# Kernel tuning notes

Measured on AMD Instinct MI355X. Metric: run time of the kernel, lower is better.

The kernel has to match this reference:

```python
import jax, jax.numpy as jnp
import numpy as np

N, IN_F, OUT_F = 8192, 512, 64
ALPHA = 0.2  # LeakyReLU negative slope


def setup_inputs() -> dict:
    key = jax.random.key(0)
    k1, k2, k3, k4 = jax.random.split(key, 4)
    x = jax.random.normal(k1, (N, IN_F), dtype=jnp.float32)
    # dense 0/1 adjacency; Bernoulli(0.5) so every row has neighbors
    adj = jax.random.randint(k2, (N, N), 0, 2, dtype=jnp.int32)
    # W stored as [in, out] (torch Linear applies x @ W.T; equivalent math)
    W = jax.random.normal(k3, (IN_F, OUT_F), dtype=jnp.float32) / np.sqrt(IN_F)
    a = jax.random.normal(k4, (2 * OUT_F,), dtype=jnp.float32) * 0.1
    return {"x": x, "adj": adj, "W": W, "a": a}


def reference(x, adj, W, a):
    # Wh: [n, out]
    Wh = x @ W
    # concat([Wh_i, Wh_j]) @ a  ==  (Wh @ a1)_i + (Wh @ a2)_j  (split 'a' in halves)
    a1, a2 = a[:OUT_F], a[OUT_F:]
    e = (Wh @ a1)[:, None] + (Wh @ a2)[None, :]          # [n, n]
    e = jnp.where(e > 0, e, ALPHA * e)                    # LeakyReLU
    e = jnp.where(adj == 0, -jnp.inf, e)                  # mask non-edges
    attn = jax.nn.softmax(e, axis=1)                      # softmax over neighbors j
    # dropout omitted: eval mode (training=False)
    return attn @ Wh                                      # [n, out]
```

## Files before the change

### kernel.cpp

```cpp
#include <hip/hip_runtime.h>
#include <cstdint>
#include <cstddef>

#define NN 8192
#define INF 512
#define OUTF 64
#define ALPHA 0.2f
#define NSPLIT 16
#define JSPLIT (NN / NSPLIT)
#define NW32 (NN / 32)
#define GEMM_BLOCKS 512

typedef short bf16x8 __attribute__((ext_vector_type(8)));
typedef float f32x4 __attribute__((ext_vector_type(4)));

static __device__ inline unsigned short f2bf(float f) {
    unsigned u = __builtin_bit_cast(unsigned, f);
    unsigned r = (u + 0x7FFFu + ((u >> 16) & 1u)) >> 16;
    return (unsigned short)r;
}

__global__ __launch_bounds__(256) void k01_fused(
    const float* __restrict__ x, const int* __restrict__ adj,
    const float* __restrict__ W, const float* __restrict__ a,
    unsigned short* __restrict__ Asw, float* __restrict__ U,
    float* __restrict__ E2p, float* __restrict__ E2n,
    unsigned* __restrict__ mask)
{
    __shared__ int ldsbuf[8192];
    const int tid = threadIdx.x;

    if (blockIdx.x >= GEMM_BLOCKS) {
        const int row = blockIdx.x - GEMM_BLOCKS;
        const int* arow = adj + (size_t)row * NN;

        #pragma unroll
        for (int k = 0; k < 8; ++k) {
            const int i = k * 1024 + tid * 4;
            int4 v = *(const int4*)(arow + i);
            const int p = i ^ (((i >> 7) & 7) << 2);
            *(int4*)&ldsbuf[p] = v;
        }
        __syncthreads();

        unsigned m = 0;
        #pragma unroll
        for (int k = 0; k < 8; ++k) {
            const int i2 = tid * 32 + k * 4;
            const int p2 = i2 ^ (((i2 >> 7) & 7) << 2);
            int4 v = *(const int4*)&ldsbuf[p2];
            m |= (v.x != 0 ? 1u : 0u) << (4 * k);
            m |= (v.y != 0 ? 1u : 0u) << (4 * k + 1);
            m |= (v.z != 0 ? 1u : 0u) << (4 * k + 2);
            m |= (v.w != 0 ? 1u : 0u) << (4 * k + 3);
        }
        mask[(size_t)row * NW32 + tid] = m;
        return;
    }

    const int i0 = blockIdx.x * 16;
    const int w  = __builtin_amdgcn_readfirstlane(tid >> 6);
    const int c  = tid & 63;

    const float* xr = x + (size_t)(i0 + 4 * w) * INF;
    const float* Wc = W + c;
    float acc[4] = {0.f, 0.f, 0.f, 0.f};

    #pragma unroll 4
    for (int kk = 0; kk < 128; ++kk) {
        const float4 x0 = *(const float4*)(xr + 0 * INF + kk * 4);
        const float4 x1 = *(const float4*)(xr + 1 * INF + kk * 4);
        const float4 x2 = *(const float4*)(xr + 2 * INF + kk * 4);
        const float4 x3 = *(const float4*)(xr + 3 * INF + kk * 4);
        const float w0 = Wc[(kk * 4 + 0) * OUTF];
        const float w1 = Wc[(kk * 4 + 1) * OUTF];
        const float w2 = Wc[(kk * 4 + 2) * OUTF];
        const float w3 = Wc[(kk * 4 + 3) * OUTF];
        acc[0] = fmaf(x0.x, w0, fmaf(x0.y, w1, fmaf(x0.z, w2, fmaf(x0.w, w3, acc[0]))));
        acc[1] = fmaf(x1.x, w0, fmaf(x1.y, w1, fmaf(x1.z, w2, fmaf(x1.w, w3, acc[1]))));
        acc[2] = fmaf(x2.x, w0, fmaf(x2.y, w1, fmaf(x2.z, w2, fmaf(x2.w, w3, acc[2]))));
        acc[3] = fmaf(x3.x, w0, fmaf(x3.y, w1, fmaf(x3.z, w2, fmaf(x3.w, w3, acc[3]))));
    }

    const float a1c = a[c];
    const float a2c = a[64 + c];
    #pragma unroll
    for (int q = 0; q < 4; ++q) {
        float v1 = acc[q] * a1c;
        float v2 = acc[q] * a2c;
        #pragma unroll
        for (int m = 32; m; m >>= 1) {
            v1 += __shfl_xor(v1, m, 64);
            v2 += __shfl_xor(v2, m, 64);
        }
        if (c == 0) {
            const int i = i0 + 4 * w + q;
            U[i]   = __expf((1.0f - ALPHA) * v1);
            E2p[i] = __expf(v2);
            E2n[i] = __expf(ALPHA * v2);
        }
    }

    const int i   = i0 + 4 * w;
    const int jt  = i >> 5;
    const int sub = (i >> 3) & 3;
    const int e0  = i & 7;
    ushort4 pk;
    pk.x = f2bf(acc[0]); pk.y = f2bf(acc[1]);
    pk.z = f2bf(acc[2]); pk.w = f2bf(acc[3]);
    *(ushort4*)&Asw[((size_t)(c >> 4) * 256 + jt) * 512 + ((c & 15) + 16 * sub) * 8 + e0] = pk;
}

__global__ __launch_bounds__(256, 4) void k2_attn(
    const unsigned* __restrict__ mask, const unsigned short* __restrict__ Asw,
    const float* __restrict__ Ug, const float* __restrict__ E2pg,
    const float* __restrict__ E2ng,
    float* __restrict__ Opart, float* __restrict__ lpart)
{
    const int l    = threadIdx.x & 63;
    const int task = blockIdx.x * 4 + (threadIdx.x >> 6);

    const int it    = task >> 4;
    const int split = task & 15;
    const int i0    = it * 32;
    const int jbase = split * JSPLIT;
    const int jb32  = jbase >> 5;

    const int il  = l & 15;
    const int kg  = l >> 4;
    const int kg8 = kg * 8;

    const float ua = Ug[i0 + il];
    const float ub = Ug[i0 + 16 + il];

    const unsigned* mbase = mask + (size_t)(i0 + il) * NW32 + jb32 + kg;
    unsigned mA[4], mB[4];
    #pragma unroll
    for (int ss = 0; ss < 4; ++ss) {
        mA[ss] = mbase[ss * 4];
        mB[ss] = mbase[(size_t)16 * NW32 + ss * 4];
    }

    f32x4 a00 = {0,0,0,0}, a01 = {0,0,0,0}, a10 = {0,0,0,0}, a11 = {0,0,0,0};
    f32x4 a20 = {0,0,0,0}, a21 = {0,0,0,0}, a30 = {0,0,0,0}, a31 = {0,0,0,0};
    float rsA = 0.f, rsB = 0.f;

    const float* ep0 = E2pg + jbase + kg8;
    const float* en0 = E2ng + jbase + kg8;

    float4 pc0 = *(const float4*)(ep0);
    float4 pc1 = *(const float4*)(ep0 + 4);
    float4 nc0 = *(const float4*)(en0);
    float4 nc1 = *(const float4*)(en0 + 4);
    unsigned bAc = (__shfl(mA[0], il, 64) >> kg8) & 0xffu;
    unsigned bBc = (__shfl(mB[0], il, 64) >> kg8) & 0xffu;

#define SCM(UU, EP, EN, BITS, K)                                              \
    ((((BITS) >> (K)) & 1u) ? fmaxf((UU) * (EP), (EN)) : 0.f)

    #pragma unroll
    for (int t = 0; t < 16; ++t) {
        const unsigned short* Ac = Asw + (size_t)(jb32 + t) * 512 + l * 8;
        bf16x8 A0c = *(const bf16x8*)(Ac);
        bf16x8 A1c = *(const bf16x8*)(Ac + 131072);
        bf16x8 A2c = *(const bf16x8*)(Ac + 262144);
        bf16x8 A3c = *(const bf16x8*)(Ac + 393216);

        const int tn = (t < 15) ? t + 1 : t;
        const float* epn = E2pg + jbase + tn * 32 + kg8;
        const float* enn = E2ng + jbase + tn * 32 + kg8;
        float4 pn0 = *(const float4*)(epn);
        float4 pn1 = *(const float4*)(epn + 4);
        float4 nn0 = *(const float4*)(enn);
        float4 nn1 = *(const float4*)(enn + 4);
        const int ssn = tn >> 2, ksn = tn & 3;
        unsigned bAn = (__shfl(mA[ssn], il + 16 * ksn, 64) >> kg8) & 0xffu;
        unsigned bBn = (__shfl(mB[ssn], il + 16 * ksn, 64) >> kg8) & 0xffu;

        const float p0 = SCM(ua, pc0.x, nc0.x, bAc, 0);
        const float p1 = SCM(ua, pc0.y, nc0.y, bAc, 1);
        const float p2 = SCM(ua, pc0.z, nc0.z, bAc, 2);
        const float p3 = SCM(ua, pc0.w, nc0.w, bAc, 3);
        const float p4 = SCM(ua, pc1.x, nc1.x, bAc, 4);
        const float p5 = SCM(ua, pc1.y, nc1.y, bAc, 5);
        const float p6 = SCM(ua, pc1.z, nc1.z, bAc, 6);
        const float p7 = SCM(ua, pc1.w, nc1.w, bAc, 7);
        const float q0 = SCM(ub, pc0.x, nc0.x, bBc, 0);
        const float q1 = SCM(ub, pc0.y, nc0.y, bBc, 1);
        const float q2 = SCM(ub, pc0.z, nc0.z, bBc, 2);
        const float q3 = SCM(ub, pc0.w, nc0.w, bBc, 3);
        const float q4 = SCM(ub, pc1.x, nc1.x, bBc, 4);
        const float q5 = SCM(ub, pc1.y, nc1.y, bBc, 5);
        const float q6 = SCM(ub, pc1.z, nc1.z, bBc, 6);
        const float q7 = SCM(ub, pc1.w, nc1.w, bBc, 7);

        rsA += ((p0 + p1) + (p2 + p3)) + ((p4 + p5) + (p6 + p7));
        rsB += ((q0 + q1) + (q2 + q3)) + ((q4 + q5) + (q6 + q7));

        uint4 wa, wb;
        asm("v_cvt_pk_bf16_f32 %0, %1, %2" : "=v"(wa.x) : "v"(p0), "v"(p1));
        asm("v_cvt_pk_bf16_f32 %0, %1, %2" : "=v"(wa.y) : "v"(p2), "v"(p3));
        asm("v_cvt_pk_bf16_f32 %0, %1, %2" : "=v"(wa.z) : "v"(p4), "v"(p5));
        asm("v_cvt_pk_bf16_f32 %0, %1, %2" : "=v"(wa.w) : "v"(p6), "v"(p7));
        asm("v_cvt_pk_bf16_f32 %0, %1, %2" : "=v"(wb.x) : "v"(q0), "v"(q1));
        asm("v_cvt_pk_bf16_f32 %0, %1, %2" : "=v"(wb.y) : "v"(q2), "v"(q3));
        asm("v_cvt_pk_bf16_f32 %0, %1, %2" : "=v"(wb.z) : "v"(q4), "v"(q5));
        asm("v_cvt_pk_bf16_f32 %0, %1, %2" : "=v"(wb.w) : "v"(q6), "v"(q7));
        const bf16x8 BA = __builtin_bit_cast(bf16x8, wa);
        const bf16x8 BB = __builtin_bit_cast(bf16x8, wb);

        a00 = __builtin_amdgcn_mfma_f32_16x16x32_bf16(A0c, BA, a00, 0, 0, 0);
        a01 = __builtin_amdgcn_mfma_f32_16x16x32_bf16(A0c, BB, a01, 0, 0, 0);
        a10 = __builtin_amdgcn_mfma_f32_16x16x32_bf16(A1c, BA, a10, 0, 0, 0);
        a11 = __builtin_amdgcn_mfma_f32_16x16x32_bf16(A1c, BB, a11, 0, 0, 0);
        a20 = __builtin_amdgcn_mfma_f32_16x16x32_bf16(A2c, BA, a20, 0, 0, 0);
        a21 = __builtin_amdgcn_mfma_f32_16x16x32_bf16(A2c, BB, a21, 0, 0, 0);
        a30 = __builtin_amdgcn_mfma_f32_16x16x32_bf16(A3c, BA, a30, 0, 0, 0);
        a31 = __builtin_amdgcn_mfma_f32_16x16x32_bf16(A3c, BB, a31, 0, 0, 0);

        pc0 = pn0; pc1 = pn1; nc0 = nn0; nc1 = nn1;
        bAc = bAn; bBc = bBn;
    }
#undef SCM

    rsA += __shfl_xor(rsA, 16, 64);
    rsA += __shfl_xor(rsA, 32, 64);
    rsB += __shfl_xor(rsB, 16, 64);
    rsB += __shfl_xor(rsB, 32, 64);
    if (l < 16) {
        lpart[(size_t)split * NN + i0 + il]      = rsA;
        lpart[(size_t)split * NN + i0 + 16 + il] = rsB;
    }

    const int nn4 = kg * 4;
    float* OA = Opart + ((size_t)split * NN + i0 + il) * OUTF + nn4;
    float* OB = OA + (size_t)16 * OUTF;
    *(float4*)(OA)      = *(float4*)&a00;
    *(float4*)(OA + 16) = *(float4*)&a10;
    *(float4*)(OA + 32) = *(float4*)&a20;
    *(float4*)(OA + 48) = *(float4*)&a30;
    *(float4*)(OB)      = *(float4*)&a01;
    *(float4*)(OB + 16) = *(float4*)&a11;
    *(float4*)(OB + 32) = *(float4*)&a21;
    *(float4*)(OB + 48) = *(float4*)&a31;
}

__global__ __launch_bounds__(256) void k3_combine(
    const float* __restrict__ Opart, const float* __restrict__ lpart,
    float* __restrict__ out)
{
    const int f4 = blockIdx.x * 256 + threadIdx.x;
    const int i  = f4 >> 4;

    float4 r = {0.f, 0.f, 0.f, 0.f};
    float  lsum = 0.f;
    #pragma unroll
    for (int s = 0; s < NSPLIT; ++s) {
        float4 o = *(const float4*)&Opart[(size_t)s * NN * OUTF + (size_t)f4 * 4];
        r.x += o.x; r.y += o.y; r.z += o.z; r.w += o.w;
        lsum += lpart[(size_t)s * NN + i];
    }
    float inv = 1.0f / lsum;
    r.x *= inv; r.y *= inv; r.z *= inv; r.w *= inv;
    *(float4*)&out[(size_t)f4 * 4] = r;
}

extern "C" void kernel_launch(void* const* d_in, const int* in_sizes, int n_in,
                              void* d_out, int out_size, void* d_ws, size_t ws_size,
                              hipStream_t stream) {
    const float* x   = (const float*)d_in[0];
    const int*   adj = (const int*)d_in[1];
    const float* W   = (const float*)d_in[2];
    const float* a   = (const float*)d_in[3];
    float* out = (float*)d_out;

    char* ws = (char*)d_ws;
    unsigned short* Asw = (unsigned short*)ws;
    float* U     = (float*)(ws + (1 << 20));
    float* E2p   = (float*)(ws + (1 << 20) + 32768);
    float* E2n   = (float*)(ws + (1 << 20) + 65536);
    float* lpart = (float*)(ws + (1 << 20) + 98304);
    unsigned* mask = (unsigned*)(ws + (1 << 20) + 98304 + 524288);
    float* Opart = (float*)(ws + (1 << 20) + 98304 + 524288 + (8 << 20));

    k01_fused<<<GEMM_BLOCKS + NN, 256, 0, stream>>>(x, adj, W, a, Asw,
                                                    U, E2p, E2n, mask);
    k2_attn<<<1024, 256, 0, stream>>>(mask, Asw, U, E2p, E2n, Opart, lpart);
    k3_combine<<<512, 256, 0, stream>>>(Opart, lpart, out);
}
```

Baseline: 91.51 us.

## Switch attention scores to packed fp16 math and compute row sums via MFMA

```diff
diff --git a/kernel.cpp b/kernel.cpp
--- a/kernel.cpp
+++ b/kernel.cpp
@@ -9,29 +9,29 @@
 #define NSPLIT 16
 #define JSPLIT (NN / NSPLIT)
 #define NW32 (NN / 32)
-#define GEMM_BLOCKS 512
-
-typedef short bf16x8 __attribute__((ext_vector_type(8)));
+
+typedef _Float16 half8 __attribute__((ext_vector_type(8)));
 typedef float f32x4 __attribute__((ext_vector_type(4)));
 
-static __device__ inline unsigned short f2bf(float f) {
-    unsigned u = __builtin_bit_cast(unsigned, f);
-    unsigned r = (u + 0x7FFFu + ((u >> 16) & 1u)) >> 16;
-    return (unsigned short)r;
+static __device__ inline unsigned short f2h(float f) {
+    _Float16 h = (_Float16)f;
+    return __builtin_bit_cast(unsigned short, h);
 }
 
 __global__ __launch_bounds__(256) void k01_fused(
     const float* __restrict__ x, const int* __restrict__ adj,
     const float* __restrict__ W, const float* __restrict__ a,
     unsigned short* __restrict__ Asw, float* __restrict__ U,
-    float* __restrict__ E2p, float* __restrict__ E2n,
+    unsigned short* __restrict__ e2ph, unsigned short* __restrict__ e2nh,
     unsigned* __restrict__ mask)
 {
     __shared__ int ldsbuf[8192];
     const int tid = threadIdx.x;
-
-    if (blockIdx.x >= GEMM_BLOCKS) {
-        const int row = blockIdx.x - GEMM_BLOCKS;
+    const int bid = blockIdx.x;
+    const int g   = bid / 17;
+
+    if (bid % 17 != 16) {
+        const int row = bid - g;
         const int* arow = adj + (size_t)row * NN;
 
         #pragma unroll
@@ -58,10 +58,9 @@
         return;
     }
 
-    const int i0 = blockIdx.x * 16;
+    const int i0 = g * 16;
     const int w  = __builtin_amdgcn_readfirstlane(tid >> 6);
     const int c  = tid & 63;
-
     const float* xr = x + (size_t)(i0 + 4 * w) * INF;
     const float* Wc = W + c;
     float acc[4] = {0.f, 0.f, 0.f, 0.f};
@@ -95,9 +94,9 @@
         }
         if (c == 0) {
             const int i = i0 + 4 * w + q;
-            U[i]   = __expf((1.0f - ALPHA) * v1);
-            E2p[i] = __expf(v2);
-            E2n[i] = __expf(ALPHA * v2);
+            U[i]    = __expf((1.0f - ALPHA) * v1);
+            e2ph[i] = f2h(__expf(v2));
+            e2nh[i] = f2h(__expf(ALPHA * v2));
         }
     }
 
@@ -106,15 +105,15 @@
     const int sub = (i >> 3) & 3;
     const int e0  = i & 7;
     ushort4 pk;
-    pk.x = f2bf(acc[0]); pk.y = f2bf(acc[1]);
-    pk.z = f2bf(acc[2]); pk.w = f2bf(acc[3]);
+    pk.x = f2h(acc[0]); pk.y = f2h(acc[1]);
+    pk.z = f2h(acc[2]); pk.w = f2h(acc[3]);
     *(ushort4*)&Asw[((size_t)(c >> 4) * 256 + jt) * 512 + ((c & 15) + 16 * sub) * 8 + e0] = pk;
 }
 
 __global__ __launch_bounds__(256, 4) void k2_attn(
     const unsigned* __restrict__ mask, const unsigned short* __restrict__ Asw,
-    const float* __restrict__ Ug, const float* __restrict__ E2pg,
-    const float* __restrict__ E2ng,
+    const float* __restrict__ Ug, const unsigned short* __restrict__ e2ph,
+    const unsigned short* __restrict__ e2nh,
     float* __restrict__ Opart, float* __restrict__ lpart)
 {
     const int l    = threadIdx.x & 63;
@@ -130,8 +129,10 @@
     const int kg  = l >> 4;
     const int kg8 = kg * 8;
 
-    const float ua = Ug[i0 + il];
-    const float ub = Ug[i0 + 16 + il];
+    const unsigned uaw = f2h(Ug[i0 + il]);
+    const unsigned ubw = f2h(Ug[i0 + 16 + il]);
+    const unsigned ua2 = uaw * 0x00010001u;
+    const unsigned ub2 = ubw * 0x00010001u;
 
     const unsigned* mbase = mask + (size_t)(i0 + il) * NW32 + jb32 + kg;
     unsigned mA[4], mB[4];
@@ -143,93 +144,73 @@
 
     f32x4 a00 = {0,0,0,0}, a01 = {0,0,0,0}, a10 = {0,0,0,0}, a11 = {0,0,0,0};
     f32x4 a20 = {0,0,0,0}, a21 = {0,0,0,0}, a30 = {0,0,0,0}, a31 = {0,0,0,0};
-    float rsA = 0.f, rsB = 0.f;
-
-    const float* ep0 = E2pg + jbase + kg8;
-    const float* en0 = E2ng + jbase + kg8;
-
-    float4 pc0 = *(const float4*)(ep0);
-    float4 pc1 = *(const float4*)(ep0 + 4);
-    float4 nc0 = *(const float4*)(en0);
-    float4 nc1 = *(const float4*)(en0 + 4);
+    f32x4 sA  = {0,0,0,0}, sB  = {0,0,0,0};
+
+    half8 ONESH;
+    #pragma unroll
+    for (int e = 0; e < 8; ++e) ONESH[e] = (_Float16)1.0f;
+
+    uint4 epc = *(const uint4*)(e2ph + jbase + kg8);
+    uint4 enc = *(const uint4*)(e2nh + jbase + kg8);
     unsigned bAc = (__shfl(mA[0], il, 64) >> kg8) & 0xffu;
     unsigned bBc = (__shfl(mB[0], il, 64) >> kg8) & 0xffu;
 
-#define SCM(UU, EP, EN, BITS, K)                                              \
-    ((((BITS) >> (K)) & 1u) ? fmaxf((UU) * (EP), (EN)) : 0.f)
+#define SPAIR(DST, U2, EPW, ENW, BITS, R) do {                                \
+    unsigned mu_, mx_;                                                        \
+    asm("v_pk_mul_f16 %0, %1, %2" : "=v"(mu_) : "v"(U2), "v"(EPW));           \
+    asm("v_pk_max_f16 %0, %1, %2" : "=v"(mx_) : "v"(mu_), "v"(ENW));          \
+    const int lo_ = (int)((BITS) << (31 - 2 * (R))) >> 31;                    \
+    const int hi_ = (int)((BITS) << (30 - 2 * (R))) >> 31;                    \
+    DST = mx_ & (((unsigned)hi_ & 0xFFFF0000u) | ((unsigned)lo_ & 0x0000FFFFu)); \
+} while (0)
 
     #pragma unroll
     for (int t = 0; t < 16; ++t) {
         const unsigned short* Ac = Asw + (size_t)(jb32 + t) * 512 + l * 8;
-        bf16x8 A0c = *(const bf16x8*)(Ac);
-        bf16x8 A1c = *(const bf16x8*)(Ac + 131072);
-        bf16x8 A2c = *(const bf16x8*)(Ac + 262144);
-        bf16x8 A3c = *(const bf16x8*)(Ac + 393216);
+        half8 A0c = *(const half8*)(Ac);
+        half8 A1c = *(const half8*)(Ac + 131072);
+        half8 A2c = *(const half8*)(Ac + 262144);
+        half8 A3c = *(const half8*)(Ac + 393216);
 
         const int tn = (t < 15) ? t + 1 : t;
-        const float* epn = E2pg + jbase + tn * 32 + kg8;
-        const float* enn = E2ng + jbase + tn * 32 + kg8;
-        float4 pn0 = *(const float4*)(epn);
-        float4 pn1 = *(const float4*)(epn + 4);
-        float4 nn0 = *(const float4*)(enn);
-        float4 nn1 = *(const float4*)(enn + 4);
+        uint4 epn = *(const uint4*)(e2ph + jbase + tn * 32 + kg8);
+        uint4 enn = *(const uint4*)(e2nh + jbase + tn * 32 + kg8);
         const int ssn = tn >> 2, ksn = tn & 3;
         unsigned bAn = (__shfl(mA[ssn], il + 16 * ksn, 64) >> kg8) & 0xffu;
         unsigned bBn = (__shfl(mB[ssn], il + 16 * ksn, 64) >> kg8) & 0xffu;
 
-        const float p0 = SCM(ua, pc0.x, nc0.x, bAc, 0);
-        const float p1 = SCM(ua, pc0.y, nc0.y, bAc, 1);
-        const float p2 = SCM(ua, pc0.z, nc0.z, bAc, 2);
-        const float p3 = SCM(ua, pc0.w, nc0.w, bAc, 3);
-        const float p4 = SCM(ua, pc1.x, nc1.x, bAc, 4);
-        const float p5 = SCM(ua, pc1.y, nc1.y, bAc, 5);
-        const float p6 = SCM(ua, pc1.z, nc1.z, bAc, 6);
-        const float p7 = SCM(ua, pc1.w, nc1.w, bAc, 7);
-        const float q0 = SCM(ub, pc0.x, nc0.x, bBc, 0);
-        const float q1 = SCM(ub, pc0.y, nc0.y, bBc, 1);
-        const float q2 = SCM(ub, pc0.z, nc0.z, bBc, 2);
-        const float q3 = SCM(ub, pc0.w, nc0.w, bBc, 3);
-        const float q4 = SCM(ub, pc1.x, nc1.x, bBc, 4);
-        const float q5 = SCM(ub, pc1.y, nc1.y, bBc, 5);
-        const float q6 = SCM(ub, pc1.z, nc1.z, bBc, 6);
-        const float q7 = SCM(ub, pc1.w, nc1.w, bBc, 7);
-
-        rsA += ((p0 + p1) + (p2 + p3)) + ((p4 + p5) + (p6 + p7));
-        rsB += ((q0 + q1) + (q2 + q3)) + ((q4 + q5) + (q6 + q7));
-
         uint4 wa, wb;
-        asm("v_cvt_pk_bf16_f32 %0, %1, %2" : "=v"(wa.x) : "v"(p0), "v"(p1));
-        asm("v_cvt_pk_bf16_f32 %0, %1, %2" : "=v"(wa.y) : "v"(p2), "v"(p3));
-        asm("v_cvt_pk_bf16_f32 %0, %1, %2" : "=v"(wa.z) : "v"(p4), "v"(p5));
-        asm("v_cvt_pk_bf16_f32 %0, %1, %2" : "=v"(wa.w) : "v"(p6), "v"(p7));
-        asm("v_cvt_pk_bf16_f32 %0, %1, %2" : "=v"(wb.x) : "v"(q0), "v"(q1));
-        asm("v_cvt_pk_bf16_f32 %0, %1, %2" : "=v"(wb.y) : "v"(q2), "v"(q3));
-        asm("v_cvt_pk_bf16_f32 %0, %1, %2" : "=v"(wb.z) : "v"(q4), "v"(q5));
-        asm("v_cvt_pk_bf16_f32 %0, %1, %2" : "=v"(wb.w) : "v"(q6), "v"(q7));
-        const bf16x8 BA = __builtin_bit_cast(bf16x8, wa);
-        const bf16x8 BB = __builtin_bit_cast(bf16x8, wb);
-
-        a00 = __builtin_amdgcn_mfma_f32_16x16x32_bf16(A0c, BA, a00, 0, 0, 0);
-        a01 = __builtin_amdgcn_mfma_f32_16x16x32_bf16(A0c, BB, a01, 0, 0, 0);
-        a10 = __builtin_amdgcn_mfma_f32_16x16x32_bf16(A1c, BA, a10, 0, 0, 0);
-        a11 = __builtin_amdgcn_mfma_f32_16x16x32_bf16(A1c, BB, a11, 0, 0, 0);
-        a20 = __builtin_amdgcn_mfma_f32_16x16x32_bf16(A2c, BA, a20, 0, 0, 0);
-        a21 = __builtin_amdgcn_mfma_f32_16x16x32_bf16(A2c, BB, a21, 0, 0, 0);
-        a30 = __builtin_amdgcn_mfma_f32_16x16x32_bf16(A3c, BA, a30, 0, 0, 0);
-        a31 = __builtin_amdgcn_mfma_f32_16x16x32_bf16(A3c, BB, a31, 0, 0, 0);
-
-        pc0 = pn0; pc1 = pn1; nc0 = nn0; nc1 = nn1;
+        SPAIR(wa.x, ua2, epc.x, enc.x, bAc, 0);
+        SPAIR(wa.y, ua2, epc.y, enc.y, bAc, 1);
+        SPAIR(wa.z, ua2, epc.z, enc.z, bAc, 2);
+        SPAIR(wa.w, ua2, epc.w, enc.w, bAc, 3);
+        SPAIR(wb.x, ub2, epc.x, enc.x, bBc, 0);
+        SPAIR(wb.y, ub2, epc.y, enc.y, bBc, 1);
+        SPAIR(wb.z, ub2, epc.z, enc.z, bBc, 2);
+        SPAIR(wb.w, ub2, epc.w, enc.w, bBc, 3);
+        const half8 BA = __builtin_bit_cast(half8, wa);
+        const half8 BB = __builtin_bit_cast(half8, wb);
+
+        sA = __builtin_amdgcn_mfma_f32_16x16x32_f16(ONESH, BA, sA, 0, 0, 0);
+        sB = __builtin_amdgcn_mfma_f32_16x16x32_f16(ONESH, BB, sB, 0, 0, 0);
+
+        a00 = __builtin_amdgcn_mfma_f32_16x16x32_f16(A0c, BA, a00, 0, 0, 0);
+        a01 = __builtin_amdgcn_mfma_f32_16x16x32_f16(A0c, BB, a01, 0, 0, 0);
+        a10 = __builtin_amdgcn_mfma_f32_16x16x32_f16(A1c, BA, a10, 0, 0, 0);
+        a11 = __builtin_amdgcn_mfma_f32_16x16x32_f16(A1c, BB, a11, 0, 0, 0);
+        a20 = __builtin_amdgcn_mfma_f32_16x16x32_f16(A2c, BA, a20, 0, 0, 0);
+        a21 = __builtin_amdgcn_mfma_f32_16x16x32_f16(A2c, BB, a21, 0, 0, 0);
+        a30 = __builtin_amdgcn_mfma_f32_16x16x32_f16(A3c, BA, a30, 0, 0, 0);
+        a31 = __builtin_amdgcn_mfma_f32_16x16x32_f16(A3c, BB, a31, 0, 0, 0);
+
+        epc = epn; enc = enn;
         bAc = bAn; bBc = bBn;
     }
-#undef SCM
-
-    rsA += __shfl_xor(rsA, 16, 64);
-    rsA += __shfl_xor(rsA, 32, 64);
-    rsB += __shfl_xor(rsB, 16, 64);
-    rsB += __shfl_xor(rsB, 32, 64);
+#undef SPAIR
+
     if (l < 16) {
-        lpart[(size_t)split * NN + i0 + il]      = rsA;
-        lpart[(size_t)split * NN + i0 + 16 + il] = rsB;
+        lpart[(size_t)split * NN + i0 + il]      = sA[0];
+        lpart[(size_t)split * NN + i0 + 16 + il] = sB[0];
     }
 
     const int nn4 = kg * 4;
@@ -277,14 +258,14 @@
     char* ws = (char*)d_ws;
     unsigned short* Asw = (unsigned short*)ws;
     float* U     = (float*)(ws + (1 << 20));
-    float* E2p   = (float*)(ws + (1 << 20) + 32768);
-    float* E2n   = (float*)(ws + (1 << 20) + 65536);
-    float* lpart = (float*)(ws + (1 << 20) + 98304);
-    unsigned* mask = (unsigned*)(ws + (1 << 20) + 98304 + 524288);
-    float* Opart = (float*)(ws + (1 << 20) + 98304 + 524288 + (8 << 20));
-
-    k01_fused<<<GEMM_BLOCKS + NN, 256, 0, stream>>>(x, adj, W, a, Asw,
-                                                    U, E2p, E2n, mask);
-    k2_attn<<<1024, 256, 0, stream>>>(mask, Asw, U, E2p, E2n, Opart, lpart);
+    unsigned short* e2ph = (unsigned short*)(ws + (1 << 20) + 32768);
+    unsigned short* e2nh = (unsigned short*)(ws + (1 << 20) + 49152);
+    float* lpart = (float*)(ws + (1 << 20) + 65536);
+    unsigned* mask = (unsigned*)(ws + (1 << 20) + 65536 + 524288);
+    float* Opart = (float*)(ws + (1 << 20) + 65536 + 524288 + (8 << 20));
+
+    k01_fused<<<512 * 17, 256, 0, stream>>>(x, adj, W, a, Asw,
+                                            U, e2ph, e2nh, mask);
+    k2_attn<<<1024, 256, 0, stream>>>(mask, Asw, U, e2ph, e2nh, Opart, lpart);
     k3_combine<<<512, 256, 0, stream>>>(Opart, lpart, out);
 }
```

After: 111.1 us. 21.5% more time.
